# Performance work log

Hardware: AMD Instinct MI355X
Metric: run time of the kernel (lower is better)

The kernel has to match this reference:

```python
import jax, jax.numpy as jnp
import numpy as np

U = 64       # LTC units / motor neurons
I = 128      # sensory (input) size
O = 15       # output_size
UNFOLDS = 4  # ode_unfolds
EPS = 1e-8   # ncps LTCCell epsilon


def setup_inputs() -> dict:
    key = jax.random.key(0)
    ks = jax.random.split(key, 16)
    B, T = 512, 512
    u = lambda k, shp, lo, hi: jax.random.uniform(k, shp, jnp.float32, lo, hi)
    sign = lambda k, shp: jnp.where(jax.random.bernoulli(k, 0.5, shp), 1.0, -1.0).astype(jnp.float32)
    return {
        "x": jax.random.normal(ks[0], (B, T, I), jnp.float32),
        # affine input mapping
        "input_w": jnp.ones((I,), jnp.float32),
        "input_b": jnp.zeros((I,), jnp.float32),
        # sensory synapses (I -> U)
        "sensory_w": u(ks[1], (I, U), 0.001, 1.0),
        "sensory_mu": u(ks[2], (I, U), 0.3, 0.8),
        "sensory_sigma": u(ks[3], (I, U), 3.0, 8.0),
        "sensory_erev": sign(ks[4], (I, U)),
        # recurrent synapses (U -> U)
        "w": u(ks[5], (U, U), 0.001, 1.0),
        "mu": u(ks[6], (U, U), 0.3, 0.8),
        "sigma": u(ks[7], (U, U), 3.0, 8.0),
        "erev": sign(ks[8], (U, U)),
        # per-neuron params
        "gleak": u(ks[9], (U,), 0.001, 1.0),
        "vleak": u(ks[10], (U,), -0.2, 0.2),
        "cm": u(ks[11], (U,), 0.4, 0.6),
        # affine output mapping
        "output_w": jnp.ones((U,), jnp.float32),
        "output_b": jnp.zeros((U,), jnp.float32),
        # LayerNorm + fc head
        "ln_w": jnp.ones((U,), jnp.float32),
        "ln_b": jnp.zeros((U,), jnp.float32),
        "fc_w": jax.random.normal(ks[12], (O, U), jnp.float32) * 0.05,
        "fc_b": jnp.zeros((O,), jnp.float32),
    }


def reference(x, input_w, input_b, sensory_w, sensory_mu, sensory_sigma, sensory_erev,
              w, mu, sigma, erev, gleak, vleak, cm, output_w, output_b,
              ln_w, ln_b, fc_w, fc_b):
    B = x.shape[0]
    sp = jax.nn.softplus
    # implicit_param_constraints=True -> softplus on w, sensory_w, gleak, cm
    w_pos = sp(w)
    sw_pos = sp(sensory_w)
    gleak_p = sp(gleak)
    cm_t = sp(cm) / (1.0 / UNFOLDS)  # elapsed_time = 1.0

    @jax.checkpoint
    def step(v, xt):
        inp = xt * input_w + input_b                                   # (B, I)
        s_act = sw_pos * jax.nn.sigmoid(sensory_sigma * (inp[:, :, None] - sensory_mu))  # (B, I, U)
        w_num_s = jnp.sum(s_act * sensory_erev, axis=1)                # (B, U)
        w_den_s = jnp.sum(s_act, axis=1)                               # (B, U)

        def unfold(v, _):
            w_act = w_pos * jax.nn.sigmoid(sigma * (v[:, :, None] - mu))  # (B, U, U)
            num = cm_t * v + gleak_p * vleak + jnp.sum(w_act * erev, axis=1) + w_num_s
            den = cm_t + gleak_p + jnp.sum(w_act, axis=1) + w_den_s
            return num / (den + EPS), None

        v, _ = jax.lax.scan(unfold, v, None, length=UNFOLDS)
        return v, None

    v0 = jnp.zeros((B, U), x.dtype)
    v_last, _ = jax.lax.scan(step, v0, jnp.swapaxes(x, 0, 1))  # scan over T
    # affine output mapping of the LTC (motor = all units for FullyConnected)
    h = v_last * output_w + output_b                               # (B, U)
    # LayerNorm (eps=1e-5) -- dropout is identity in eval
    mean = jnp.mean(h, axis=-1, keepdims=True)
    var = jnp.var(h, axis=-1, keepdims=True)
    h = (h - mean) * jax.lax.rsqrt(var + 1e-5) * ln_w + ln_b
    return h @ fc_w.T + fc_b                                       # (B, O)
```

## Files before the change

kernel.cpp:

```cpp
#include <hip/hip_runtime.h>
#include <hip/hip_bf16.h>


#define NB 512
#define NT 512
#define NI 128
#define NU 64
#define NO 15
#define L2E 1.44269504088896340736f

__device__ __forceinline__ float bcastf(float v, int lane) {
  return __int_as_float(__builtin_amdgcn_readlane(__float_as_int(v), lane));
}

__device__ __forceinline__ float wsum64(float x) {
#pragma unroll
  for (int m = 32; m >= 1; m >>= 1) x += __shfl_xor(x, m, 64);
  return x;
}

__device__ __forceinline__ float softplus_f(float x) {
  return log1pf(expf(x));
}

__device__ __forceinline__ float sigm_term(float a, float vb, float c) {
  float z = fmaf(a, vb, c);
  float e = __builtin_amdgcn_exp2f(z);
  return __builtin_amdgcn_rcpf(1.0f + e);
}

__global__ __launch_bounds__(256, 2) void ltc_fused(
    const float* __restrict__ x,
    const float* __restrict__ input_w, const float* __restrict__ input_b,
    const float* __restrict__ sensory_w, const float* __restrict__ sensory_mu,
    const float* __restrict__ sensory_sigma, const float* __restrict__ sensory_erev,
    const float* __restrict__ w_, const float* __restrict__ mu_,
    const float* __restrict__ sigma_, const float* __restrict__ erev_,
    const float* __restrict__ gleak, const float* __restrict__ vleak,
    const float* __restrict__ cm,
    const float* __restrict__ output_w, const float* __restrict__ output_b,
    const float* __restrict__ ln_w, const float* __restrict__ ln_b,
    const float* __restrict__ fc_w, const float* __restrict__ fc_b,
    float* __restrict__ out)
{
  const int b    = blockIdx.x;
  const int tid  = threadIdx.x;
  const int wv   = tid >> 6;
  const int lane = tid & 63;

  __shared__ float2 xbuf[4][4][NU];

  float sa[32], sc[32], swe[32], swp[32];
#pragma unroll
  for (int k = 0; k < 32; ++k) {
    const int idx = (32 * wv + k) * NU + lane;
    const float ss = sensory_sigma[idx];
    const float sm = sensory_mu[idx];
    const float sw = softplus_f(sensory_w[idx]);
    const float se = sensory_erev[idx];
    sa[k]  = -L2E * ss;
    sc[k]  =  L2E * ss * sm;
    swe[k] = sw * se;
    swp[k] = sw;
  }
  float ra[16], rc[16], rwe[16], rwp[16];
#pragma unroll
  for (int k = 0; k < 16; ++k) {
    const int idx = (16 * wv + k) * NU + lane;
    const float sg = sigma_[idx];
    const float m  = mu_[idx];
    const float ww = softplus_f(w_[idx]);
    const float ev = erev_[idx];
    ra[k]  = -L2E * sg;
    rc[k]  =  L2E * sg * m;
    rwe[k] = ww * ev;
    rwp[k] = ww;
  }

  const float glp   = softplus_f(gleak[lane]);
  const float cmt   = softplus_f(cm[lane]) * 4.0f;
  const float glvl  = glp * vleak[lane];
  const float dbase = cmt + glp;

  const int ii = 32 * wv + (lane & 31);
  const float iw = input_w[ii];
  const float ib = input_b[ii];

  float v = 0.0f;
  const float* xp = x + (size_t)b * NT * NI + ii;
  float xv = xp[0];

#pragma unroll 1
  for (int t = 0; t < NT; ++t) {
    const int tn = (t + 1 < NT) ? (t + 1) : t;
    const float xv_next = xp[(size_t)tn * NI];
    const float inp = fmaf(xv, iw, ib);

    float ns0=0.f, ns1=0.f, ns2=0.f, ns3=0.f;
    float ds0=0.f, ds1=0.f, ds2=0.f, ds3=0.f;
#pragma unroll
    for (int k = 0; k < 32; k += 4) {
      { float s = sigm_term(sa[k+0], bcastf(inp, k+0), sc[k+0]);
        ns0 = fmaf(swe[k+0], s, ns0); ds0 = fmaf(swp[k+0], s, ds0); }
      { float s = sigm_term(sa[k+1], bcastf(inp, k+1), sc[k+1]);
        ns1 = fmaf(swe[k+1], s, ns1); ds1 = fmaf(swp[k+1], s, ds1); }
      { float s = sigm_term(sa[k+2], bcastf(inp, k+2), sc[k+2]);
        ns2 = fmaf(swe[k+2], s, ns2); ds2 = fmaf(swp[k+2], s, ds2); }
      { float s = sigm_term(sa[k+3], bcastf(inp, k+3), sc[k+3]);
        ns3 = fmaf(swe[k+3], s, ns3); ds3 = fmaf(swp[k+3], s, ds3); }
    }
    const float wns = (ns0 + ns1) + (ns2 + ns3);
    const float wds = (ds0 + ds1) + (ds2 + ds3);

#pragma unroll
    for (int u = 0; u < 4; ++u) {
      float rn0=0.f, rn1=0.f, rn2=0.f, rn3=0.f;
      float rd0=0.f, rd1=0.f, rd2=0.f, rd3=0.f;
      const int i0 = 16 * wv;
#pragma unroll
      for (int k = 0; k < 16; k += 4) {
        { float s = sigm_term(ra[k+0], bcastf(v, i0+k+0), rc[k+0]);
          rn0 = fmaf(rwe[k+0], s, rn0); rd0 = fmaf(rwp[k+0], s, rd0); }
        { float s = sigm_term(ra[k+1], bcastf(v, i0+k+1), rc[k+1]);
          rn1 = fmaf(rwe[k+1], s, rn1); rd1 = fmaf(rwp[k+1], s, rd1); }
        { float s = sigm_term(ra[k+2], bcastf(v, i0+k+2), rc[k+2]);
          rn2 = fmaf(rwe[k+2], s, rn2); rd2 = fmaf(rwp[k+2], s, rd2); }
        { float s = sigm_term(ra[k+3], bcastf(v, i0+k+3), rc[k+3]);
          rn3 = fmaf(rwe[k+3], s, rn3); rd3 = fmaf(rwp[k+3], s, rd3); }
      }
      const float np = ((rn0 + rn1) + (rn2 + rn3)) + wns;
      const float dp = ((rd0 + rd1) + (rd2 + rd3)) + wds;
      xbuf[u][wv][lane] = make_float2(np, dp);
      __syncthreads();
      const float2 p0 = xbuf[u][0][lane];
      const float2 p1 = xbuf[u][1][lane];
      const float2 p2 = xbuf[u][2][lane];
      const float2 p3 = xbuf[u][3][lane];
      const float num = fmaf(cmt, v, glvl) + ((p0.x + p1.x) + (p2.x + p3.x));
      const float den = dbase + ((p0.y + p1.y) + (p2.y + p3.y)) + 1e-8f;
      v = num * __builtin_amdgcn_rcpf(den);
    }
    xv = xv_next;
  }

  if (wv == 0) {
    const float h    = fmaf(v, output_w[lane], output_b[lane]);
    const float mean = wsum64(h) * (1.0f / 64.0f);
    const float d    = h - mean;
    const float var  = wsum64(d * d) * (1.0f / 64.0f);
    const float hn   = d * rsqrtf(var + 1e-5f) * ln_w[lane] + ln_b[lane];
#pragma unroll
    for (int o = 0; o < NO; ++o) {
      const float p = wsum64(hn * fc_w[o * NU + lane]);
      if (lane == 0) out[b * NO + o] = p + fc_b[o];
    }
  }
}

extern "C" void kernel_launch(void* const* d_in, const int* in_sizes, int n_in,
                              void* d_out, int out_size, void* d_ws, size_t ws_size,
                              hipStream_t stream) {
  const float* x             = (const float*)d_in[0];
  const float* input_w       = (const float*)d_in[1];
  const float* input_b       = (const float*)d_in[2];
  const float* sensory_w     = (const float*)d_in[3];
  const float* sensory_mu    = (const float*)d_in[4];
  const float* sensory_sigma = (const float*)d_in[5];
  const float* sensory_erev  = (const float*)d_in[6];
  const float* w_            = (const float*)d_in[7];
  const float* mu_           = (const float*)d_in[8];
  const float* sigma_        = (const float*)d_in[9];
  const float* erev_         = (const float*)d_in[10];
  const float* gleak         = (const float*)d_in[11];
  const float* vleak         = (const float*)d_in[12];
  const float* cm            = (const float*)d_in[13];
  const float* output_w      = (const float*)d_in[14];
  const float* output_b      = (const float*)d_in[15];
  const float* ln_w          = (const float*)d_in[16];
  const float* ln_b          = (const float*)d_in[17];
  const float* fc_w          = (const float*)d_in[18];
  const float* fc_b          = (const float*)d_in[19];
  float* out = (float*)d_out;

  ltc_fused<<<dim3(NB), dim3(256), 0, stream>>>(
      x, input_w, input_b, sensory_w, sensory_mu, sensory_sigma, sensory_erev,
      w_, mu_, sigma_, erev_, gleak, vleak, cm, output_w, output_b,
      ln_w, ln_b, fc_w, fc_b, out);
}
```

Baseline: 2.173 ms.

## Split each batch row over eight waves, batch reciprocals, and pack accumulators

Each block now runs 512 threads (8 waves) instead of 256, so each wave handles 16 sensory and 8 recurrent input rows instead of 32 and 16. This cuts the serial per-wave chain between barriers and lowers register pressure. Four sigmoid reciprocals are merged into one rcp plus multiplies, with clamping on the sensory exponent to avoid overflow in the product. Numerator and denominator are accumulated as float2 vectors so they can use packed FMA. The cost is an 8-way LDS reduction at each unfold step and barriers that now span more waves.

```diff
diff --git a/kernel.cpp b/kernel.cpp
--- a/kernel.cpp
+++ b/kernel.cpp
@@ -8,6 +8,8 @@
 #define NU 64
 #define NO 15
 #define L2E 1.44269504088896340736f
+
+typedef float v2f __attribute__((ext_vector_type(2)));
 
 __device__ __forceinline__ float bcastf(float v, int lane) {
   return __int_as_float(__builtin_amdgcn_readlane(__float_as_int(v), lane));
@@ -23,13 +25,20 @@
   return log1pf(expf(x));
 }
 
-__device__ __forceinline__ float sigm_term(float a, float vb, float c) {
-  float z = fmaf(a, vb, c);
-  float e = __builtin_amdgcn_exp2f(z);
-  return __builtin_amdgcn_rcpf(1.0f + e);
+__device__ __forceinline__ void sig4(float z0, float z1, float z2, float z3,
+                                     float& s0, float& s1, float& s2, float& s3) {
+  const float e0 = __builtin_amdgcn_exp2f(z0);
+  const float e1 = __builtin_amdgcn_exp2f(z1);
+  const float e2 = __builtin_amdgcn_exp2f(z2);
+  const float e3 = __builtin_amdgcn_exp2f(z3);
+  const float A = 1.0f + e0, B = 1.0f + e1, C = 1.0f + e2, D = 1.0f + e3;
+  const float pAB = A * B, pCD = C * D;
+  const float r = __builtin_amdgcn_rcpf(pAB * pCD);
+  const float rAB = r * pCD, rCD = r * pAB;
+  s0 = rAB * B; s1 = rAB * A; s2 = rCD * D; s3 = rCD * C;
 }
 
-__global__ __launch_bounds__(256, 2) void ltc_fused(
+__global__ __launch_bounds__(512, 4) void ltc_fused(
     const float* __restrict__ x,
     const float* __restrict__ input_w, const float* __restrict__ input_b,
     const float* __restrict__ sensory_w, const float* __restrict__ sensory_mu,
@@ -48,41 +57,41 @@
   const int wv   = tid >> 6;
   const int lane = tid & 63;
 
-  __shared__ float2 xbuf[4][4][NU];
+  __shared__ v2f xbuf[4][8][NU];
 
-  float sa[32], sc[32], swe[32], swp[32];
+  float sa[16], sc[16];
+  v2f   sw2[16];
 #pragma unroll
-  for (int k = 0; k < 32; ++k) {
-    const int idx = (32 * wv + k) * NU + lane;
+  for (int k = 0; k < 16; ++k) {
+    const int idx = (16 * wv + k) * NU + lane;
     const float ss = sensory_sigma[idx];
     const float sm = sensory_mu[idx];
     const float sw = softplus_f(sensory_w[idx]);
     const float se = sensory_erev[idx];
-    sa[k]  = -L2E * ss;
-    sc[k]  =  L2E * ss * sm;
-    swe[k] = sw * se;
-    swp[k] = sw;
+    sa[k] = -L2E * ss;
+    sc[k] =  L2E * ss * sm;
+    sw2[k] = (v2f){sw * se, sw};
   }
-  float ra[16], rc[16], rwe[16], rwp[16];
+  float ra[8], rc[8];
+  v2f   rw2[8];
 #pragma unroll
-  for (int k = 0; k < 16; ++k) {
-    const int idx = (16 * wv + k) * NU + lane;
+  for (int k = 0; k < 8; ++k) {
+    const int idx = (8 * wv + k) * NU + lane;
     const float sg = sigma_[idx];
     const float m  = mu_[idx];
     const float ww = softplus_f(w_[idx]);
     const float ev = erev_[idx];
-    ra[k]  = -L2E * sg;
-    rc[k]  =  L2E * sg * m;
-    rwe[k] = ww * ev;
-    rwp[k] = ww;
+    ra[k] = -L2E * sg;
+    rc[k] =  L2E * sg * m;
+    rw2[k] = (v2f){ww * ev, ww};
   }
 
   const float glp   = softplus_f(gleak[lane]);
   const float cmt   = softplus_f(cm[lane]) * 4.0f;
   const float glvl  = glp * vleak[lane];
-  const float dbase = cmt + glp;
+  const float dbase = cmt + glp + 1e-8f;
 
-  const int ii = 32 * wv + (lane & 31);
+  const int ii = 16 * wv + (lane & 15);
   const float iw = input_w[ii];
   const float ib = input_b[ii];
 
@@ -96,48 +105,49 @@
     const float xv_next = xp[(size_t)tn * NI];
     const float inp = fmaf(xv, iw, ib);
 
-    float ns0=0.f, ns1=0.f, ns2=0.f, ns3=0.f;
-    float ds0=0.f, ds1=0.f, ds2=0.f, ds3=0.f;
+    v2f sens = (v2f){0.0f, 0.0f};
 #pragma unroll
-    for (int k = 0; k < 32; k += 4) {
-      { float s = sigm_term(sa[k+0], bcastf(inp, k+0), sc[k+0]);
-        ns0 = fmaf(swe[k+0], s, ns0); ds0 = fmaf(swp[k+0], s, ds0); }
-      { float s = sigm_term(sa[k+1], bcastf(inp, k+1), sc[k+1]);
-        ns1 = fmaf(swe[k+1], s, ns1); ds1 = fmaf(swp[k+1], s, ds1); }
-      { float s = sigm_term(sa[k+2], bcastf(inp, k+2), sc[k+2]);
-        ns2 = fmaf(swe[k+2], s, ns2); ds2 = fmaf(swp[k+2], s, ds2); }
-      { float s = sigm_term(sa[k+3], bcastf(inp, k+3), sc[k+3]);
-        ns3 = fmaf(swe[k+3], s, ns3); ds3 = fmaf(swp[k+3], s, ds3); }
+    for (int k = 0; k < 16; k += 4) {
+      float z0 = fmaf(sa[k+0], bcastf(inp, k+0), sc[k+0]);
+      float z1 = fmaf(sa[k+1], bcastf(inp, k+1), sc[k+1]);
+      float z2 = fmaf(sa[k+2], bcastf(inp, k+2), sc[k+2]);
+      float z3 = fmaf(sa[k+3], bcastf(inp, k+3), sc[k+3]);
+      z0 = fminf(fmaxf(z0, -30.0f), 30.0f);
+      z1 = fminf(fmaxf(z1, -30.0f), 30.0f);
+      z2 = fminf(fmaxf(z2, -30.0f), 30.0f);
+      z3 = fminf(fmaxf(z3, -30.0f), 30.0f);
+      float s0, s1, s2, s3;
+      sig4(z0, z1, z2, z3, s0, s1, s2, s3);
+      sens += sw2[k+0] * (v2f){s0, s0};
+      sens += sw2[k+1] * (v2f){s1, s1};
+      sens += sw2[k+2] * (v2f){s2, s2};
+      sens += sw2[k+3] * (v2f){s3, s3};
     }
-    const float wns = (ns0 + ns1) + (ns2 + ns3);
-    const float wds = (ds0 + ds1) + (ds2 + ds3);
 
 #pragma unroll
     for (int u = 0; u < 4; ++u) {
-      float rn0=0.f, rn1=0.f, rn2=0.f, rn3=0.f;
-      float rd0=0.f, rd1=0.f, rd2=0.f, rd3=0.f;
-      const int i0 = 16 * wv;
+      const int i0 = 8 * wv;
+      v2f acc = sens;
 #pragma unroll
-      for (int k = 0; k < 16; k += 4) {
-        { float s = sigm_term(ra[k+0], bcastf(v, i0+k+0), rc[k+0]);
-          rn0 = fmaf(rwe[k+0], s, rn0); rd0 = fmaf(rwp[k+0], s, rd0); }
-        { float s = sigm_term(ra[k+1], bcastf(v, i0+k+1), rc[k+1]);
-          rn1 = fmaf(rwe[k+1], s, rn1); rd1 = fmaf(rwp[k+1], s, rd1); }
-        { float s = sigm_term(ra[k+2], bcastf(v, i0+k+2), rc[k+2]);
-          rn2 = fmaf(rwe[k+2], s, rn2); rd2 = fmaf(rwp[k+2], s, rd2); }
-        { float s = sigm_term(ra[k+3], bcastf(v, i0+k+3), rc[k+3]);
-          rn3 = fmaf(rwe[k+3], s, rn3); rd3 = fmaf(rwp[k+3], s, rd3); }
+      for (int k = 0; k < 8; k += 4) {
+        const float z0 = fmaf(ra[k+0], bcastf(v, i0+k+0), rc[k+0]);
+        const float z1 = fmaf(ra[k+1], bcastf(v, i0+k+1), rc[k+1]);
+        const float z2 = fmaf(ra[k+2], bcastf(v, i0+k+2), rc[k+2]);
+        const float z3 = fmaf(ra[k+3], bcastf(v, i0+k+3), rc[k+3]);
+        float s0, s1, s2, s3;
+        sig4(z0, z1, z2, z3, s0, s1, s2, s3);
+        acc += rw2[k+0] * (v2f){s0, s0};
+        acc += rw2[k+1] * (v2f){s1, s1};
+        acc += rw2[k+2] * (v2f){s2, s2};
+        acc += rw2[k+3] * (v2f){s3, s3};
       }
-      const float np = ((rn0 + rn1) + (rn2 + rn3)) + wns;
-      const float dp = ((rd0 + rd1) + (rd2 + rd3)) + wds;
-      xbuf[u][wv][lane] = make_float2(np, dp);
+      xbuf[u][wv][lane] = acc;
       __syncthreads();
-      const float2 p0 = xbuf[u][0][lane];
-      const float2 p1 = xbuf[u][1][lane];
-      const float2 p2 = xbuf[u][2][lane];
-      const float2 p3 = xbuf[u][3][lane];
-      const float num = fmaf(cmt, v, glvl) + ((p0.x + p1.x) + (p2.x + p3.x));
-      const float den = dbase + ((p0.y + p1.y) + (p2.y + p3.y)) + 1e-8f;
+      v2f tot = xbuf[u][0][lane];
+#pragma unroll
+      for (int p = 1; p < 8; ++p) tot += xbuf[u][p][lane];
+      const float num = fmaf(cmt, v, glvl) + tot.x;
+      const float den = dbase + tot.y;
       v = num * __builtin_amdgcn_rcpf(den);
     }
     xv = xv_next;
@@ -182,7 +192,7 @@
   const float* fc_b          = (const float*)d_in[19];
   float* out = (float*)d_out;
 
-  ltc_fused<<<dim3(NB), dim3(256), 0, stream>>>(
+  ltc_fused<<<dim3(NB), dim3(512), 0, stream>>>(
       x, input_w, input_b, sensory_w, sensory_mu, sensory_sigma, sensory_erev,
       w_, mu_, sigma_, erev_, gleak, vleak, cm, output_w, output_b,
       ln_w, ln_b, fc_w, fc_b, out);
```

After: 2.402 ms. 1.11x slower.
